# Kernel optimization log

Measured on AMD Instinct MI355X. Metric: run time of the kernel, lower is better.

Reference implementation:

```python
import jax, jax.numpy as jnp
import numpy as np

B, S, E = 2, 2048, 1024
H = 16
D = E // H  # head dim

def setup_inputs() -> dict:
    key = jax.random.key(0)
    ks = jax.random.split(key, 9)
    s = 1.0 / np.sqrt(E)
    return {
        "hidden_states": jax.random.normal(ks[0], (B, S, E), dtype=jnp.float32),
        "Wq": jax.random.normal(ks[1], (E, E), dtype=jnp.float32) * s,
        "bq": jnp.zeros((E,), jnp.float32),
        "Wk": jax.random.normal(ks[2], (E, E), dtype=jnp.float32) * s,
        "bk": jnp.zeros((E,), jnp.float32),
        "Wv": jax.random.normal(ks[3], (E, E), dtype=jnp.float32) * s,
        "bv": jnp.zeros((E,), jnp.float32),
        "Wo": jax.random.normal(ks[4], (E, E), dtype=jnp.float32) * s,
        "bo": jnp.zeros((E,), jnp.float32),
    }

def _split_heads(x):
    # [B,S,E] -> [B,H,S,D]
    b, s, _ = x.shape
    return x.reshape(b, s, H, D).transpose(0, 2, 1, 3)

def reference(hidden_states, Wq, bq, Wk, bk, Wv, bv, Wo, bo):
    q = _split_heads(hidden_states @ Wq + bq)  # [B,H,S,D]
    k = _split_heads(hidden_states @ Wk + bk)
    v = _split_heads(hidden_states @ Wv + bv)
    scores = jnp.einsum('bhqd,bhkd->bhqk', q, k) / jnp.sqrt(jnp.float32(D))
    probs = jax.nn.softmax(scores, axis=-1)  # [B,H,S,S]
    ctx = jnp.einsum('bhqk,bhkd->bhqd', probs, v)
    ctx = ctx.transpose(0, 2, 1, 3).reshape(hidden_states.shape[0], -1, E)
    out = ctx @ Wo + bo
    return out, probs
```

## Files before the change

### kernel.cpp

```cpp
#include <hip/hip_runtime.h>
#include <hip/hip_bf16.h>
#include <stdint.h>


typedef __attribute__((ext_vector_type(8))) short bf16x8;
typedef __attribute__((ext_vector_type(4))) short bf16x4v;
typedef __attribute__((ext_vector_type(4))) float f32x4;

#define DEV static __device__ __forceinline__

DEV short f2bs(float f) {
  union { __hip_bfloat16 b; short s; } u;
  u.b = __float2bfloat16(f);
  return u.s;
}
DEV f32x4 mfma16(bf16x8 a, bf16x8 b, f32x4 c) {
  return __builtin_amdgcn_mfma_f32_16x16x32_bf16(a, b, c, 0, 0, 0);
}
DEV float fexp2(float x) { return __builtin_amdgcn_exp2f(x); }
typedef const __attribute__((address_space(1))) void* gas1_t;
typedef __attribute__((address_space(3))) void* las3_t;
DEV void gload_lds16(const void* g, void* l) {
  __builtin_amdgcn_global_load_lds((gas1_t)(uintptr_t)g, (las3_t)(uint32_t)(uintptr_t)l,
                                   16, 0, 0);
}
#define WAIT_VMCNT(N) asm volatile("s_waitcnt vmcnt(" #N ")" ::: "memory")
#define WAIT_LGKM0() asm volatile("s_waitcnt lgkmcnt(0)" ::: "memory")
#define BARRIER() do { __builtin_amdgcn_s_barrier(); __builtin_amdgcn_sched_barrier(0); } while (0)

__global__ void cvt_all_kernel(const float* __restrict__ X,
                               const float* __restrict__ Wq, const float* __restrict__ Wk,
                               const float* __restrict__ Wv, const float* __restrict__ Wo,
                               short* __restrict__ Xb, short* __restrict__ Wt) {
  __shared__ short tile[64][68];
  int bx = blockIdx.x, t = threadIdx.x;
  if (bx < 2048) {
    size_t i = (size_t)bx * 256 + t;
    const float4* X4 = (const float4*)X;
    float4 a = X4[2 * i], c = X4[2 * i + 1];
    bf16x8 o;
    o[0] = f2bs(a.x); o[1] = f2bs(a.y); o[2] = f2bs(a.z); o[3] = f2bs(a.w);
    o[4] = f2bs(c.x); o[5] = f2bs(c.y); o[6] = f2bs(c.z); o[7] = f2bs(c.w);
    *(bf16x8*)(Xb + i * 8) = o;
    return;
  }
  int wb = bx - 2048;
  int mat = wb >> 8, rem = wb & 255;
  const float* W = mat == 0 ? Wq : mat == 1 ? Wk : mat == 2 ? Wv : Wo;
  int kb = (rem >> 4) * 64, nb = (rem & 15) * 64;
#pragma unroll
  for (int it = 0; it < 4; ++it) {
    int idx = it * 256 + t;
    int row = idx >> 4, c4 = (idx & 15) * 4;
    float4 v = *(const float4*)(W + (size_t)(kb + row) * 1024 + nb + c4);
    tile[row][c4 + 0] = f2bs(v.x); tile[row][c4 + 1] = f2bs(v.y);
    tile[row][c4 + 2] = f2bs(v.z); tile[row][c4 + 3] = f2bs(v.w);
  }
  __syncthreads();
#pragma unroll
  for (int it = 0; it < 4; ++it) {
    int idx = it * 256 + t;
    int rn = idx >> 4, c4 = (idx & 15) * 4;
    bf16x4v o;
    o[0] = tile[c4 + 0][rn]; o[1] = tile[c4 + 1][rn];
    o[2] = tile[c4 + 2][rn]; o[3] = tile[c4 + 3][rn];
    *(bf16x4v*)(Wt + (((size_t)mat) << 20) + (size_t)(nb + rn) * 1024 + kb + c4) = o;
  }
}

template <int MODE>
__global__ __launch_bounds__(256, 2)
void gemm_bt_kernel(const short* __restrict__ A, const short* __restrict__ Bt,
                    const float* __restrict__ bias0, const float* __restrict__ bias1,
                    const float* __restrict__ bias2,
                    short* __restrict__ o0, short* __restrict__ o1, short* __restrict__ o2,
                    float* __restrict__ fout) {
  __shared__ short As[128 * 32];
  __shared__ short Bs[128 * 32];
  const int m0 = blockIdx.x * 128, n0 = blockIdx.y * 128;
  const int t = threadIdx.x, w = t >> 6, l = t & 63, g = l >> 4, r = l & 15;
  const int wr = (w >> 1) * 64, wc = (w & 1) * 64;
  f32x4 acc[4][4] = {};
  for (int k0 = 0; k0 < 1024; k0 += 32) {
    gload_lds16(A + (size_t)(m0 + (t >> 2)) * 1024 + k0 + (t & 3) * 8, As + w * 512);
    gload_lds16(A + (size_t)(m0 + 64 + (t >> 2)) * 1024 + k0 + (t & 3) * 8, As + 2048 + w * 512);
    gload_lds16(Bt + (size_t)(n0 + (t >> 2)) * 1024 + k0 + (t & 3) * 8, Bs + w * 512);
    gload_lds16(Bt + (size_t)(n0 + 64 + (t >> 2)) * 1024 + k0 + (t & 3) * 8, Bs + 2048 + w * 512);
    __syncthreads();
    bf16x8 af[4], bfv[4];
#pragma unroll
    for (int i = 0; i < 4; i++) af[i] = *(const bf16x8*)(As + (wr + i * 16 + r) * 32 + g * 8);
#pragma unroll
    for (int j = 0; j < 4; j++) bfv[j] = *(const bf16x8*)(Bs + (wc + j * 16 + r) * 32 + g * 8);
#pragma unroll
    for (int i = 0; i < 4; i++)
#pragma unroll
      for (int j = 0; j < 4; j++) acc[i][j] = mfma16(af[i], bfv[j], acc[i][j]);
    __syncthreads();
  }
  if constexpr (MODE == 0) {
#pragma unroll
    for (int j = 0; j < 4; j++) {
      int ng = n0 + wc + j * 16 + r;
      int mat = ng >> 10, nn = ng & 1023, hh = nn >> 6, dd = nn & 63;
      const float* bp = mat == 0 ? bias0 : (mat == 1 ? bias1 : bias2);
      short* dst = mat == 0 ? o0 : (mat == 1 ? o1 : o2);
      float bv = bp[nn];
      float sc = (mat == 0) ? 0.18033688f : 1.0f;
#pragma unroll
      for (int i = 0; i < 4; i++) {
#pragma unroll
        for (int q = 0; q < 4; q++) {
          int m = m0 + wr + i * 16 + g * 4 + q;
          int bb = m >> 11, ss = m & 2047;
          dst[((size_t)(bb * 16 + hh) * 2048 + ss) * 64 + dd] = f2bs((acc[i][j][q] + bv) * sc);
        }
      }
    }
  } else {
#pragma unroll
    for (int i = 0; i < 4; i++)
#pragma unroll
      for (int q = 0; q < 4; q++) {
        int m = m0 + wr + i * 16 + g * 4 + q;
#pragma unroll
        for (int j = 0; j < 4; j++) {
          int ng = n0 + wc + j * 16 + r;
          fout[(size_t)m * 1024 + ng] = acc[i][j][q] + bias0[ng];
        }
      }
  }
}

__global__ __launch_bounds__(256, 4)
void attn_kernel(const short* __restrict__ Qm, const short* __restrict__ Km,
                 const short* __restrict__ Vm, float* __restrict__ probs,
                 short* __restrict__ ctx) {
  __shared__ short Ks[2][64 * 64];
  __shared__ short Vt[64 * 72];
  __shared__ short Ps[4][16 * 72];
  __shared__ float rls[64];
  const int f = blockIdx.x;
  const int wgid = (f & 7) * 128 + (f >> 3);
  const int bh = wgid >> 5, q0 = (wgid & 31) * 64;
  const int bb = bh >> 4, hh = bh & 15;
  const short* Qp = Qm + (size_t)bh * 2048 * 64;
  const short* Kp = Km + (size_t)bh * 2048 * 64;
  const short* Vp = Vm + (size_t)bh * 2048 * 64;
  float* Pp = probs + (size_t)bh * 2048 * 2048;
  const int t = threadIdx.x, w = t >> 6, l = t & 63, g = l >> 4, r = l & 15;
  const int lr = l >> 3, lc = l & 7;
  const int swz = lc ^ lr;

#define STAGE_K(kt_, buf_)                                                         \
  do {                                                                             \
    const short* src_ = Kp + (size_t)((kt_) * 64) * 64;                            \
    gload_lds16(src_ + (size_t)(w * 8 + lr) * 64 + swz * 8, Ks[buf_] + (w * 8) * 64); \
    gload_lds16(src_ + (size_t)(32 + w * 8 + lr) * 64 + swz * 8,                   \
                Ks[buf_] + (32 + w * 8) * 64);                                     \
  } while (0)

  short* Qs = &Ks[0][0];
#pragma unroll
  for (int it = 0; it < 2; ++it)
    gload_lds16(Qp + (size_t)(q0 + it * 32 + w * 8 + lr) * 64 + swz * 8,
                Qs + (it * 32 + w * 8) * 64);
  __syncthreads();
  bf16x8 qf[2];
#pragma unroll
  for (int df = 0; df < 2; df++)
    qf[df] = *(const bf16x8*)(Qs + (w * 16 + r) * 64 + ((df * 4 + g) ^ (r & 7)) * 8);
  WAIT_LGKM0();
  BARRIER();

  float lrow = 0.f;
  STAGE_K(0, 0);
  for (int kt = 0; kt < 32; ++kt) {
    const int cur = kt & 1;
    if (kt < 31) {
      STAGE_K(kt + 1, cur ^ 1);
      WAIT_VMCNT(2);
    } else {
      WAIT_VMCNT(0);
    }
    BARRIER();
    f32x4 st[4] = {};
    __builtin_amdgcn_s_setprio(1);
#pragma unroll
    for (int df = 0; df < 2; ++df) {
      bf16x8 kf[4];
#pragma unroll
      for (int ni = 0; ni < 4; ni++)
        kf[ni] = *(const bf16x8*)(Ks[cur] + (ni * 16 + r) * 64 + ((df * 4 + g) ^ (r & 7)) * 8);
#pragma unroll
      for (int ni = 0; ni < 4; ni++) st[ni] = mfma16(kf[ni], qf[df], st[ni]);
    }
    __builtin_amdgcn_s_setprio(0);
    float ssum = 0.f;
#pragma unroll
    for (int ni = 0; ni < 4; ni++)
#pragma unroll
      for (int q4 = 0; q4 < 4; q4++) ssum += fexp2(st[ni][q4]);
    ssum += __shfl_xor(ssum, 16);
    ssum += __shfl_xor(ssum, 32);
    lrow += ssum;
    BARRIER();
  }
  const float rinv = 1.0f / lrow;
  if (g == 0) rls[w * 16 + r] = rinv;

  f32x4 cacc[4] = {};
  const int kp = (t >> 3) * 2, d0v = (t & 7) * 8, lcv = t & 7, kunit = t >> 5;
  STAGE_K(0, 0);
  for (int kt = 0; kt < 32; ++kt) {
    const int cur = kt & 1;
    bf16x8 v0 = *(const bf16x8*)(Vp + (size_t)(kt * 64 + kp) * 64 + d0v);
    bf16x8 v1 = *(const bf16x8*)(Vp + (size_t)(kt * 64 + kp + 1) * 64 + d0v);
    if (kt < 31) STAGE_K(kt + 1, cur ^ 1);
    if (kt == 0) { WAIT_VMCNT(4); }
    else if (kt < 31) { WAIT_VMCNT(8); }
    else { WAIT_VMCNT(6); }
    BARRIER();
    f32x4 st[4] = {};
    __builtin_amdgcn_s_setprio(1);
#pragma unroll
    for (int df = 0; df < 2; ++df) {
      bf16x8 kf[4];
#pragma unroll
      for (int ni = 0; ni < 4; ni++)
        kf[ni] = *(const bf16x8*)(Ks[cur] + (ni * 16 + r) * 64 + ((df * 4 + g) ^ (r & 7)) * 8);
#pragma unroll
      for (int ni = 0; ni < 4; ni++) st[ni] = mfma16(kf[ni], qf[df], st[ni]);
    }
    __builtin_amdgcn_s_setprio(0);
#pragma unroll
    for (int ni = 0; ni < 4; ni++) {
      bf16x4v pk;
#pragma unroll
      for (int q4 = 0; q4 < 4; q4++) {
        float pe = fexp2(st[ni][q4]);
        st[ni][q4] = pe;
        pk[q4] = f2bs(pe);
      }
      *(bf16x4v*)(&Ps[w][r * 72 + ni * 16 + g * 4]) = pk;
    }
#pragma unroll
    for (int e = 0; e < 8; e++) {
      unsigned int pkv = (unsigned int)(unsigned short)v0[e] |
                         ((unsigned int)(unsigned short)v1[e] << 16);
      *(unsigned int*)(Vt + (d0v + e) * 72 + ((kunit ^ lcv) << 3) + (kp & 7)) = pkv;
    }
    WAIT_LGKM0();
    BARRIER();
#pragma unroll
    for (int ni = 0; ni < 4; ni++) {
      f32x4 pr;
#pragma unroll
      for (int q4 = 0; q4 < 4; q4++) pr[q4] = st[ni][q4] * rinv;
      *(f32x4*)(Pp + (size_t)(q0 + w * 16 + r) * 2048 + kt * 64 + ni * 16 + g * 4) = pr;
    }
    __builtin_amdgcn_s_setprio(1);
#pragma unroll
    for (int kf4 = 0; kf4 < 2; ++kf4) {
      bf16x8 pa, vb[4];
      pa = *(const bf16x8*)(&Ps[w][r * 72 + kf4 * 32 + g * 8]);
#pragma unroll
      for (int nj = 0; nj < 4; nj++)
        vb[nj] = *(const bf16x8*)(Vt + (nj * 16 + r) * 72 +
                                  (((kf4 * 4 + g) ^ (nj * 2 + (r >> 3))) << 3));
#pragma unroll
      for (int nj = 0; nj < 4; nj++) cacc[nj] = mfma16(pa, vb[nj], cacc[nj]);
    }
    __builtin_amdgcn_s_setprio(0);
  }
#pragma unroll
  for (int nj = 0; nj < 4; nj++)
#pragma unroll
    for (int q4 = 0; q4 < 4; q4++) {
      int qt = w * 16 + g * 4 + q4;
      float val = cacc[nj][q4] * rls[qt];
      ctx[((size_t)(bb * 2048 + q0 + qt)) * 1024 + hh * 64 + nj * 16 + r] = f2bs(val);
    }
#undef STAGE_K
}

extern "C" void kernel_launch(void* const* d_in, const int* in_sizes, int n_in,
                              void* d_out, int out_size, void* d_ws, size_t ws_size,
                              hipStream_t stream) {
  (void)in_sizes; (void)n_in; (void)out_size; (void)ws_size;
  const float* X  = (const float*)d_in[0];
  const float* Wq = (const float*)d_in[1];
  const float* bq = (const float*)d_in[2];
  const float* Wk = (const float*)d_in[3];
  const float* bk = (const float*)d_in[4];
  const float* Wv = (const float*)d_in[5];
  const float* bv = (const float*)d_in[6];
  const float* Wo = (const float*)d_in[7];
  const float* bo = (const float*)d_in[8];
  float* out = (float*)d_out;
  float* probs = out + (size_t)2 * 2048 * 1024;

  short* Xb = (short*)d_ws;
  short* Wt = Xb + (size_t)4194304;
  short* Qb = Wt + (size_t)4194304;
  short* Kb = Qb + (size_t)4194304;
  short* Vb = Kb + (size_t)4194304;
  short* Cx = Vb + (size_t)4194304;

  cvt_all_kernel<<<3072, 256, 0, stream>>>(X, Wq, Wk, Wv, Wo, Xb, Wt);
  gemm_bt_kernel<0><<<dim3(32, 24), 256, 0, stream>>>(Xb, Wt, bq, bk, bv, Qb, Kb, Vb, nullptr);
  attn_kernel<<<1024, 256, 0, stream>>>(Qb, Kb, Vb, probs, Cx);
  gemm_bt_kernel<1><<<dim3(32, 8), 256, 0, stream>>>(Cx, Wt + (size_t)3 * 1048576, bo,
                                                     nullptr, nullptr, nullptr, nullptr,
                                                     nullptr, out);
}
```

Before: 255.1 us.

## Double-buffer GEMM LDS tiles, remap blocks across XCDs, nontemporal prob stores

The projection GEMM now keeps two LDS buffers and issues the global-to-LDS loads for the next K slice before computing the current one, so load latency can overlap with MFMA work. A vmcnt wait and barriers replace the old synchronisation. Workgroup IDs are remapped so consecutive tiles land on the same XCD for better L2 reuse. The large fp32 probability matrix writes use nontemporal stores to reduce cache pollution. The cost is doubled GEMM LDS use, which may lower occupancy.

```diff
diff --git a/kernel.cpp b/kernel.cpp
--- a/kernel.cpp
+++ b/kernel.cpp
@@ -68,36 +68,58 @@
   }
 }
 
-template <int MODE>
+template <int MODE, int GBX>
 __global__ __launch_bounds__(256, 2)
 void gemm_bt_kernel(const short* __restrict__ A, const short* __restrict__ Bt,
                     const float* __restrict__ bias0, const float* __restrict__ bias1,
                     const float* __restrict__ bias2,
                     short* __restrict__ o0, short* __restrict__ o1, short* __restrict__ o2,
                     float* __restrict__ fout) {
-  __shared__ short As[128 * 32];
-  __shared__ short Bs[128 * 32];
-  const int m0 = blockIdx.x * 128, n0 = blockIdx.y * 128;
+  __shared__ short As[2][128 * 32];
+  __shared__ short Bs[2][128 * 32];
+  const int nwg = GBX * gridDim.y;
+  const int cpx = nwg >> 3;
+  const int bid0 = blockIdx.y * GBX + blockIdx.x;
+  const int bid = (bid0 % 8) * cpx + bid0 / 8;
+  const int m0 = (bid % GBX) * 128, n0 = (bid / GBX) * 128;
   const int t = threadIdx.x, w = t >> 6, l = t & 63, g = l >> 4, r = l & 15;
   const int wr = (w >> 1) * 64, wc = (w & 1) * 64;
   f32x4 acc[4][4] = {};
-  for (int k0 = 0; k0 < 1024; k0 += 32) {
-    gload_lds16(A + (size_t)(m0 + (t >> 2)) * 1024 + k0 + (t & 3) * 8, As + w * 512);
-    gload_lds16(A + (size_t)(m0 + 64 + (t >> 2)) * 1024 + k0 + (t & 3) * 8, As + 2048 + w * 512);
-    gload_lds16(Bt + (size_t)(n0 + (t >> 2)) * 1024 + k0 + (t & 3) * 8, Bs + w * 512);
-    gload_lds16(Bt + (size_t)(n0 + 64 + (t >> 2)) * 1024 + k0 + (t & 3) * 8, Bs + 2048 + w * 512);
-    __syncthreads();
+
+#define STAGE_G(k0_, b_)                                                                   \
+  do {                                                                                     \
+    gload_lds16(A + (size_t)(m0 + (t >> 2)) * 1024 + (k0_) + (t & 3) * 8, As[b_] + w * 512); \
+    gload_lds16(A + (size_t)(m0 + 64 + (t >> 2)) * 1024 + (k0_) + (t & 3) * 8,             \
+                As[b_] + 2048 + w * 512);                                                  \
+    gload_lds16(Bt + (size_t)(n0 + (t >> 2)) * 1024 + (k0_) + (t & 3) * 8, Bs[b_] + w * 512); \
+    gload_lds16(Bt + (size_t)(n0 + 64 + (t >> 2)) * 1024 + (k0_) + (t & 3) * 8,            \
+                Bs[b_] + 2048 + w * 512);                                                  \
+  } while (0)
+
+  STAGE_G(0, 0);
+  for (int it = 0; it < 32; ++it) {
+    const int cur = it & 1;
+    if (it < 31) {
+      STAGE_G((it + 1) * 32, cur ^ 1);
+      WAIT_VMCNT(4);
+    } else {
+      WAIT_VMCNT(0);
+    }
+    BARRIER();
     bf16x8 af[4], bfv[4];
 #pragma unroll
-    for (int i = 0; i < 4; i++) af[i] = *(const bf16x8*)(As + (wr + i * 16 + r) * 32 + g * 8);
-#pragma unroll
-    for (int j = 0; j < 4; j++) bfv[j] = *(const bf16x8*)(Bs + (wc + j * 16 + r) * 32 + g * 8);
+    for (int i = 0; i < 4; i++) af[i] = *(const bf16x8*)(As[cur] + (wr + i * 16 + r) * 32 + g * 8);
+#pragma unroll
+    for (int j = 0; j < 4; j++) bfv[j] = *(const bf16x8*)(Bs[cur] + (wc + j * 16 + r) * 32 + g * 8);
+    __builtin_amdgcn_s_setprio(1);
 #pragma unroll
     for (int i = 0; i < 4; i++)
 #pragma unroll
       for (int j = 0; j < 4; j++) acc[i][j] = mfma16(af[i], bfv[j], acc[i][j]);
-    __syncthreads();
-  }
+    __builtin_amdgcn_s_setprio(0);
+    BARRIER();
+  }
+#undef STAGE_G
   if constexpr (MODE == 0) {
 #pragma unroll
     for (int j = 0; j < 4; j++) {
@@ -257,7 +279,8 @@
       f32x4 pr;
 #pragma unroll
       for (int q4 = 0; q4 < 4; q4++) pr[q4] = st[ni][q4] * rinv;
-      *(f32x4*)(Pp + (size_t)(q0 + w * 16 + r) * 2048 + kt * 64 + ni * 16 + g * 4) = pr;
+      __builtin_nontemporal_store(
+          pr, (f32x4*)(Pp + (size_t)(q0 + w * 16 + r) * 2048 + kt * 64 + ni * 16 + g * 4));
     }
     __builtin_amdgcn_s_setprio(1);
 #pragma unroll
@@ -308,9 +331,10 @@
   short* Cx = Vb + (size_t)4194304;
 
   cvt_all_kernel<<<3072, 256, 0, stream>>>(X, Wq, Wk, Wv, Wo, Xb, Wt);
-  gemm_bt_kernel<0><<<dim3(32, 24), 256, 0, stream>>>(Xb, Wt, bq, bk, bv, Qb, Kb, Vb, nullptr);
+  gemm_bt_kernel<0, 32><<<dim3(32, 24), 256, 0, stream>>>(Xb, Wt, bq, bk, bv,
+                                                          Qb, Kb, Vb, nullptr);
   attn_kernel<<<1024, 256, 0, stream>>>(Qb, Kb, Vb, probs, Cx);
-  gemm_bt_kernel<1><<<dim3(32, 8), 256, 0, stream>>>(Cx, Wt + (size_t)3 * 1048576, bo,
-                                                     nullptr, nullptr, nullptr, nullptr,
-                                                     nullptr, out);
-}
+  gemm_bt_kernel<1, 32><<<dim3(32, 8), 256, 0, stream>>>(Cx, Wt + (size_t)3 * 1048576, bo,
+                                                         nullptr, nullptr, nullptr, nullptr,
+                                                         nullptr, out);
+}
```

New measurement: 259.4 us. Within noise of the previous version (+1.7%).
